# Optimization experiments

Measured on AMD Instinct MI355X. Metric: run time of the kernel, lower is better.

Reference implementation:

```python
import jax, jax.numpy as jnp
import numpy as np

NETWORK_MAP = {'DMN': [34, 35, 66, 67, 64, 65, 22, 23, 24, 25], 'SMN': [0, 1, 56, 57, 68, 69], 'VN': [42, 43, 44, 45, 46, 47, 48, 49, 50, 51, 52, 53], 'SN': [28, 29, 30, 31, 32, 33], 'FPN': [6, 7, 58, 59, 60, 61], 'LN': [36, 37, 38, 39, 40, 41], 'VAN': [10, 11, 14, 15], 'BGN': [70, 71, 72, 73, 74, 75, 76, 77], 'CereN': list(range(90, 116))}
N, K, B, IN_DIM, HID, HEADS = 116, 9, 512, 123, 128, 4
FLAT = K * HID + HID  # 1280


def _pool_mat():
    P = np.zeros((N, K), np.float32)
    for k, idxs in enumerate(NETWORK_MAP.values()):
        P[np.array(idxs), k] = 1.0
    return jnp.asarray(P)


def _bn(x, g, b, m, v):
    # eval-mode BatchNorm1d with running stats
    return (x - m) / jnp.sqrt(v + 1e-5) * g + b


def _gat(h, adj, W, a, g, bt, m, v):
    Bb, Nn, _ = h.shape
    H = a.shape[0]
    D = a.shape[1] // 2  # head_dim
    Wh = (h @ W).reshape(Bb, Nn, H, D)
    # additive GAT score factorization: (cat([Wh_i, Wh_j]) * a).sum(-1) = ei + ej
    ei = jnp.einsum('bnhd,hd->bnh', Wh, a[:, :D])
    ej = jnp.einsum('bnhd,hd->bnh', Wh, a[:, D:])
    e = ei[:, :, None, :] + ej[:, None, :, :]          # [B,N,N,H]
    e = jnp.where(e > 0, e, 0.2 * e)                   # leaky_relu(0.2)
    e = jnp.where((adj == 0)[..., None], -jnp.inf, e)  # mask non-edges
    attn = jax.nn.softmax(e, axis=2)                   # over neighbors j
    out = jnp.einsum('bijh,bjhd->bihd', attn, Wh).reshape(Bb, Nn, -1)
    out = _bn(out, g, bt, m, v)
    return jax.nn.elu(out) + h @ W


def setup_inputs() -> dict:
    key = jax.random.key(0)
    ks = jax.random.split(key, 24)
    f32 = jnp.float32

    def lin(k, fi, fo):
        return jax.random.normal(k, (fi, fo), f32) / np.sqrt(fi)

    x = jax.random.normal(ks[0], (B, N, IN_DIM), f32)
    adj = jax.random.randint(ks[1], (B, N, N), 0, 2).astype(f32)
    adj = jnp.maximum(adj, jnp.eye(N, dtype=f32)[None])  # self-loops
    return {
        'x': x, 'adj': adj,
        'W_enc': lin(ks[2], IN_DIM, HID), 'b_enc': jnp.zeros((HID,), f32),
        'bn_in_g': 1.0 + 0.1 * jax.random.normal(ks[3], (HID,), f32),
        'bn_in_b': 0.1 * jax.random.normal(ks[4], (HID,), f32),
        'bn_in_m': 0.05 * jax.random.normal(ks[5], (HID,), f32),
        'bn_in_v': jax.random.uniform(ks[6], (HID,), f32, 0.5, 1.5),
        'vne': 0.02 * jax.random.normal(ks[7], (1, 1, HID), f32),
        'W1': lin(ks[8], HID, HID),
        'a1': 0.1 * jax.random.normal(ks[9], (HEADS, 2 * (HID // HEADS)), f32),
        'g1': 1.0 + 0.1 * jax.random.normal(ks[10], (HID,), f32),
        'bt1': 0.1 * jax.random.normal(ks[11], (HID,), f32),
        'm1': 0.05 * jax.random.normal(ks[12], (HID,), f32),
        'v1': jax.random.uniform(ks[13], (HID,), f32, 0.5, 1.5),
        'W2': lin(ks[14], HID, HID),
        'a2': 0.1 * jax.random.normal(ks[15], (HEADS, 2 * (HID // HEADS)), f32),
        'g2': 1.0 + 0.1 * jax.random.normal(ks[16], (HID,), f32),
        'bt2': 0.1 * jax.random.normal(ks[17], (HID,), f32),
        'm2': 0.05 * jax.random.normal(ks[18], (HID,), f32),
        'v2': jax.random.uniform(ks[19], (HID,), f32, 0.5, 1.5),
        'Wv': lin(ks[20], 2 * HID, HID), 'bv': jnp.zeros((HID,), f32),
        'pool_mat': _pool_mat(),
        'Wa1': lin(ks[21], HID, 32), 'ba1': jnp.zeros((32,), f32),
        'Wa2': lin(ks[22], 32, 1), 'ba2': jnp.zeros((1,), f32),
        'ln_g': jnp.ones((FLAT,), f32), 'ln_b': jnp.zeros((FLAT,), f32),
        'Wc1': lin(ks[23], FLAT, 256), 'bc1': jnp.zeros((256,), f32),
        'Wc2': lin(jax.random.fold_in(key, 99), 256, 2), 'bc2': jnp.zeros((2,), f32),
    }


def reference(x, adj, W_enc, b_enc, bn_in_g, bn_in_b, bn_in_m, bn_in_v, vne,
              W1, a1, g1, bt1, m1, v1, W2, a2, g2, bt2, m2, v2,
              Wv, bv, pool_mat, Wa1, ba1, Wa2, ba2, ln_g, ln_b,
              Wc1, bc1, Wc2, bc2):
    Bb = x.shape[0]
    h = jax.nn.elu(x @ W_enc + b_enc)                 # node_encoder (dropout=eval)
    h = _bn(h, bn_in_g, bn_in_b, bn_in_m, bn_in_v)
    vn = vne + h.mean(axis=1, keepdims=True)          # [B,1,HID]
    h = _gat(h, adj, W1, a1, g1, bt1, m1, v1)
    vn_new = jax.nn.elu(jnp.concatenate([vn, h.mean(axis=1, keepdims=True)], -1) @ Wv + bv)
    h = h + vn_new * 0.1
    h2 = _gat(h, adj, W2, a2, g2, bt2, m2, v2)
    h = h2 + h
    vn = jax.nn.elu(jnp.concatenate([vn_new, h.mean(axis=1, keepdims=True)], -1) @ Wv + bv)
    pooled = jnp.einsum('bnd,nk->bkd', h, pool_mat)   # virtual-network pooling [B,K,HID]
    s = jnp.tanh(pooled @ Wa1 + ba1) @ Wa2 + ba2      # [B,K,1]
    net_w = jax.nn.softmax(s, axis=1)
    pooled = pooled * net_w
    flat = jnp.concatenate([pooled.reshape(Bb, -1), vn[:, 0]], axis=1)  # [B,FLAT]
    mu = flat.mean(axis=-1, keepdims=True)
    var = flat.var(axis=-1, keepdims=True)
    flat = (flat - mu) / jnp.sqrt(var + 1e-5) * ln_g + ln_b  # LayerNorm
    logits = jax.nn.elu(flat @ Wc1 + bc1) @ Wc2 + bc2        # classifier (dropout=eval)
    return (logits, flat)
```

## Files before the change

kernel.cpp:

```cpp
#include <hip/hip_runtime.h>
#include <hip/hip_bf16.h>
#include <math.h>

#define BATCH 512
#define N_NODES 116
#define IN_DIM 123
#define HID 128
#define HEADS 4
#define FLAT_DIM 1280

static constexpr int BN_TOT = BATCH * N_NODES;
static constexpr int HROW = N_NODES * HID;
static constexpr int ADJROW = N_NODES * N_NODES;

typedef short short8 __attribute__((ext_vector_type(8)));
typedef float f32x16 __attribute__((ext_vector_type(16)));

__device__ __forceinline__ float elu1(float x) {
    return x > 0.f ? x : __expf(x) - 1.f;
}
__device__ __forceinline__ short bfb(float x) {
    __hip_bfloat16 b = __float2bfloat16(x);
    return *reinterpret_cast<short*>(&b);
}

__global__ __launch_bounds__(256) void xprep_kernel(
    const float* __restrict__ x, short* __restrict__ xb)
{
    const int idx = blockIdx.x * 256 + threadIdx.x;
    const int row = idx >> 7, k = idx & 127;
    xb[idx] = (k < IN_DIM) ? bfb(x[(size_t)row * IN_DIM + k]) : (short)0;
}

__global__ __launch_bounds__(256) void wencprep_kernel(
    const float* __restrict__ W, short* __restrict__ Wb)
{
    const int idx = blockIdx.x * 256 + threadIdx.x;
    const int col = idx >> 7, k = idx & 127;
    Wb[idx] = (k < IN_DIM) ? bfb(W[(size_t)k * HID + col]) : (short)0;
}

__global__ __launch_bounds__(256) void enc_mfma(
    const short* __restrict__ xb, const short* __restrict__ Wencb,
    const float* __restrict__ bias,
    const float* __restrict__ g, const float* __restrict__ bta,
    const float* __restrict__ mn, const float* __restrict__ vr,
    float* __restrict__ hout)
{
    const int t = threadIdx.x;
    const int lane = t & 63, w = t >> 6;
    const int half = lane >> 5, nn = lane & 31;
    const int row0 = blockIdx.x * 128 + w * 32;
    const short8* ap = reinterpret_cast<const short8*>(xb + (size_t)(row0 + nn) * 128);
    short8 af[8];
#pragma unroll
    for (int s = 0; s < 8; ++s) af[s] = ap[s * 2 + half];
#pragma unroll
    for (int ct = 0; ct < 4; ++ct) {
        const int col = ct * 32 + nn;
        const short8* bp = reinterpret_cast<const short8*>(Wencb + (size_t)col * 128);
        f32x16 acc = {};
#pragma unroll
        for (int s = 0; s < 8; ++s)
            acc = __builtin_amdgcn_mfma_f32_32x32x16_bf16(af[s], bp[s * 2 + half], acc, 0, 0, 0);
        const float bb = bias[col];
        const float gg = g[col], bbn = bta[col], mm = mn[col];
        const float rstd = rsqrtf(vr[col] + 1e-5f);
#pragma unroll
        for (int reg = 0; reg < 16; ++reg) {
            const int r = (reg & 3) + 8 * (reg >> 2) + 4 * half;
            float val = elu1(acc[reg] + bb);
            val = (val - mm) * rstd * gg + bbn;
            hout[(size_t)(row0 + r) * HID + col] = val;
        }
    }
}

__global__ __launch_bounds__(256) void wprep_kernel(
    const float* __restrict__ W, const float* __restrict__ a,
    short* __restrict__ Wt, short* __restrict__ Weij)
{
    const int idx = blockIdx.x * 256 + threadIdx.x;
    const int h = idx >> 12, nn = (idx >> 7) & 31, k = idx & 127;
    Wt[idx] = bfb(W[k * HID + h * 32 + nn]);
    short wv = 0;
    if (nn < 2) {
        const float* ap = a + h * 64 + nn * 32;
        float s = 0.f;
#pragma unroll 8
        for (int d = 0; d < 32; ++d) s += W[k * HID + h * 32 + d] * ap[d];
        wv = bfb(s);
    }
    Weij[idx] = wv;
}

__global__ __launch_bounds__(256) void wc1prep_kernel(
    const float* __restrict__ Wc1, short* __restrict__ wc1t)
{
    const int idx = blockIdx.x * 256 + threadIdx.x;
    const int k = idx >> 8, n = idx & 255;
    wc1t[(size_t)n * FLAT_DIM + k] = bfb(Wc1[(size_t)k * 256 + n]);
}

__global__ __launch_bounds__(256) void adjpack_kernel(
    const float* __restrict__ adj, unsigned int* __restrict__ adjp)
{
    const int row = blockIdx.x * 4 + (threadIdx.x >> 6);
    const int l = threadIdx.x & 63;
    const float a1 = adj[(size_t)row * N_NODES + l];
    const float a2 = (l < N_NODES - 64) ? adj[(size_t)row * N_NODES + 64 + l] : 0.f;
    const unsigned long long m1 = __ballot(a1 != 0.f);
    const unsigned long long m2 = __ballot(a2 != 0.f);
    if (l == 0) {
        uint4 v;
        v.x = (unsigned int)m1; v.y = (unsigned int)(m1 >> 32);
        v.z = (unsigned int)m2; v.w = (unsigned int)(m2 >> 32);
        *reinterpret_cast<uint4*>(&adjp[(size_t)row * 4]) = v;
    }
}

template <bool ADD_H>
__global__ __launch_bounds__(256, 4) void gat_fused(
    const float* __restrict__ hin, float* __restrict__ hout,
    const short* __restrict__ Wt, const short* __restrict__ Weij,
    const unsigned int* __restrict__ adjp,
    const float* __restrict__ g, const float* __restrict__ bta,
    const float* __restrict__ mn, const float* __restrict__ vr,
    const float* __restrict__ vn, float* __restrict__ premean)
{
    constexpr int KP = 136;
    constexpr int WP = 33;
    __shared__ __align__(16) __hip_bfloat16 s_p[N_NODES][KP];
    __shared__ __align__(16) __hip_bfloat16 s_whsb[128][WP];
    __shared__ float s_eir[232];

    const int t = threadIdx.x;
    const int n_ = blockIdx.x;
    const int b = (n_ & 7) * 64 + (n_ >> 5);
    const int h = (n_ >> 3) & 3;

    const int lane = t & 63, w = t >> 6;
    const int half = lane >> 5, nn = lane & 31;

    {
        const int row = w * 32 + nn;
        const int hr = (row < N_NODES) ? row : 0;
        const float* hrow = hin + ((size_t)b * N_NODES + hr) * HID;
        const short8* wtp = reinterpret_cast<const short8*>(Wt + ((h * 32 + nn) << 7));
        const short8* wep = reinterpret_cast<const short8*>(Weij + ((h * 32 + nn) << 7));
        f32x16 wacc = {};
        f32x16 eacc = {};
#pragma unroll
        for (int s = 0; s < 8; ++s) {
            const int k0 = s * 16 + half * 8;
            float av[8];
            *reinterpret_cast<float4*>(&av[0]) = *reinterpret_cast<const float4*>(&hrow[k0]);
            *reinterpret_cast<float4*>(&av[4]) = *reinterpret_cast<const float4*>(&hrow[k0 + 4]);
            if (ADD_H) {
                float4 v0 = *reinterpret_cast<const float4*>(&vn[(size_t)b * HID + k0]);
                float4 v1 = *reinterpret_cast<const float4*>(&vn[(size_t)b * HID + k0 + 4]);
                av[0] += 0.1f * v0.x; av[1] += 0.1f * v0.y;
                av[2] += 0.1f * v0.z; av[3] += 0.1f * v0.w;
                av[4] += 0.1f * v1.x; av[5] += 0.1f * v1.y;
                av[6] += 0.1f * v1.z; av[7] += 0.1f * v1.w;
            }
            short8 afrag;
#pragma unroll
            for (int e = 0; e < 8; ++e) afrag[e] = bfb(av[e]);
            const int fi = s * 2 + half;
            wacc = __builtin_amdgcn_mfma_f32_32x32x16_bf16(afrag, wtp[fi], wacc, 0, 0, 0);
            eacc = __builtin_amdgcn_mfma_f32_32x32x16_bf16(afrag, wep[fi], eacc, 0, 0, 0);
        }
#pragma unroll
        for (int reg = 0; reg < 16; ++reg) {
            const int r = (reg & 3) + 8 * (reg >> 2) + 4 * half;
            s_whsb[w * 32 + r][nn] = __float2bfloat16(wacc[reg]);
        }
        if (nn == 0) {
#pragma unroll
            for (int reg = 0; reg < 16; ++reg) {
                const int r = w * 32 + (reg & 3) + 8 * (reg >> 2) + 4 * half;
                if (r < N_NODES) s_eir[r] = eacc[reg];
            }
        }
        if (nn == 1) {
#pragma unroll
            for (int reg = 0; reg < 16; ++reg) {
                const int r = w * 32 + (reg & 3) + 8 * (reg >> 2) + 4 * half;
                if (r < N_NODES) s_eir[N_NODES + r] = eacc[reg];
            }
        }
    }
    __syncthreads();

    {
        const int l = lane;
        const float ejl = s_eir[N_NODES + l];
        const bool up = (l < N_NODES - 64);
        const float ejl2 = up ? s_eir[N_NODES + l + 64] : 0.f;
        const int i0 = w * 32;
        const int cnt = min(32, N_NODES - i0);
        const uint4* ap = reinterpret_cast<const uint4*>(
            adjp + ((size_t)b * N_NODES + i0) * 4);
        uint4 aw = ap[0];
        for (int ii = 0; ii < cnt; ++ii) {
            uint4 nw = aw;
            if (ii + 1 < cnt) nw = ap[ii + 1];
            const int i = i0 + ii;
            const float eii = s_eir[i];
            const unsigned int w1 = (l & 32) ? aw.y : aw.x;
            const unsigned int w2 = (l & 32) ? aw.w : aw.z;
            const bool bit1 = (w1 >> (l & 31)) & 1;
            const bool bit2 = (w2 >> (l & 31)) & 1;
            float e1 = eii + ejl;
            e1 = e1 > 0.f ? e1 : 0.2f * e1;
            const float x1 = bit1 ? __expf(e1) : 0.f;
            float x2 = 0.f;
            if (up) {
                float e2 = eii + ejl2;
                e2 = e2 > 0.f ? e2 : 0.2f * e2;
                x2 = bit2 ? __expf(e2) : 0.f;
            }
            s_p[i][l] = __float2bfloat16(x1);
            s_p[i][l + 64] = __float2bfloat16(x2);
            aw = nw;
        }
    }

    float psum = 0.f;
    {
        f32x16 acc = {};
        f32x16 accs = {};
        short8 ones;
#pragma unroll
        for (int e = 0; e < 8; ++e) ones[e] = (short)0x3F80;
#pragma unroll
        for (int s = 0; s < 8; ++s) {
            const int k0 = s * 16 + half * 8;
            const short8 afrag = *reinterpret_cast<const short8*>(
                &s_p[0][0] + (size_t)(w * 32 + nn) * KP + k0);
            short8 bfrag;
#pragma unroll
            for (int e = 0; e < 8; ++e)
                bfrag[e] = *reinterpret_cast<const short*>(&s_whsb[k0 + e][nn]);
            acc = __builtin_amdgcn_mfma_f32_32x32x16_bf16(afrag, bfrag, acc, 0, 0, 0);
            accs = __builtin_amdgcn_mfma_f32_32x32x16_bf16(afrag, ones, accs, 0, 0, 0);
        }
        const int f = h * 32 + nn;
        const float gg = g[f], bb = bta[f], mm = mn[f];
        const float rstd = rsqrtf(vr[f] + 1e-5f);
        const float vadd = ADD_H ? 0.1f * vn[(size_t)b * HID + f] : 0.f;
#pragma unroll
        for (int reg = 0; reg < 16; ++reg) {
            const int row = (reg & 3) + 8 * (reg >> 2) + 4 * half;
            const int i = w * 32 + row;
            if (i < N_NODES) {
                const size_t off = ((size_t)b * N_NODES + i) * HID + f;
                const float aval = acc[reg] / accs[reg];
                float xv = elu1((aval - mm) * rstd * gg + bb);
                float outv = xv + __bfloat162float(s_whsb[i][nn]);
                if (ADD_H) outv += hin[off] + vadd;
                hout[off] = outv;
                psum += outv;
            }
        }
    }
    psum += __shfl_xor(psum, 32);
    __syncthreads();
    if (half == 0) s_eir[w * 32 + nn] = psum;
    __syncthreads();
    if (t < 32) {
        const float s = s_eir[t] + s_eir[32 + t] + s_eir[64 + t] + s_eir[96 + t];
        premean[(size_t)b * HID + h * 32 + t] = s * (1.f / N_NODES);
    }
}

__global__ __launch_bounds__(128) void vn0_kernel(
    const float* __restrict__ h, const float* __restrict__ vne,
    float* __restrict__ vn)
{
    const int b = blockIdx.x, f = threadIdx.x;
    float s = 0.f;
    for (int n = 0; n < N_NODES; ++n) s += h[(size_t)b * HROW + n * HID + f];
    vn[b * HID + f] = vne[f] + s * (1.f / N_NODES);
}

__global__ __launch_bounds__(128) void vn_mlp_kernel(
    const float* __restrict__ prev, const float* __restrict__ premean,
    const float* __restrict__ Wv, const float* __restrict__ bv,
    float* __restrict__ vout)
{
    __shared__ float cat[2 * HID];
    const int b = blockIdx.x, f = threadIdx.x;
    cat[f] = prev[b * HID + f];
    cat[HID + f] = premean[b * HID + f];
    __syncthreads();
    float acc = bv[f];
    for (int k = 0; k < 2 * HID; ++k) acc += cat[k] * Wv[k * HID + f];
    vout[b * HID + f] = elu1(acc);
}

__global__ __launch_bounds__(128) void pool_flat_kernel(
    const float* __restrict__ h, const float* __restrict__ vnf,
    const float* __restrict__ pm,
    const float* __restrict__ Wa1, const float* __restrict__ ba1,
    const float* __restrict__ Wa2, const float* __restrict__ ba2,
    const float* __restrict__ ln_g, const float* __restrict__ ln_b,
    float* __restrict__ out, short* __restrict__ flatb)
{
    __shared__ float s_pm[N_NODES * 9];
    __shared__ float s_p[9][HID];
    __shared__ float s_s[9];
    __shared__ float s_red[4];
    const int b = blockIdx.x, f = threadIdx.x;
    for (int idx = f; idx < N_NODES * 9; idx += 128) s_pm[idx] = pm[idx];
    float p[9] = {};
    __syncthreads();
    for (int n = 0; n < N_NODES; ++n) {
        const float hv = h[(size_t)b * HROW + n * HID + f];
#pragma unroll
        for (int k = 0; k < 9; ++k) p[k] += s_pm[n * 9 + k] * hv;
    }
#pragma unroll
    for (int k = 0; k < 9; ++k) s_p[k][f] = p[k];
    __syncthreads();
    for (int pass = 0; pass < 3; ++pass) {
        const int k = pass * 4 + (f >> 5);
        if (k < 9) {
            const int j = f & 31;
            float z = ba1[j];
            for (int d = 0; d < HID; ++d) z += s_p[k][d] * Wa1[d * 32 + j];
            z = tanhf(z);
            float part = z * Wa2[j];
#pragma unroll
            for (int off = 16; off; off >>= 1) part += __shfl_xor(part, off);
            if (j == 0) s_s[k] = part + ba2[0];
        }
    }
    __syncthreads();
    float smax = -1e30f;
#pragma unroll
    for (int k = 0; k < 9; ++k) smax = fmaxf(smax, s_s[k]);
    float wgt[9], ssum = 0.f;
#pragma unroll
    for (int k = 0; k < 9; ++k) { wgt[k] = expf(s_s[k] - smax); ssum += wgt[k]; }
    const float sinv = 1.f / ssum;
    float vals[10];
#pragma unroll
    for (int k = 0; k < 9; ++k) vals[k] = p[k] * wgt[k] * sinv;
    vals[9] = vnf[b * HID + f];
    float lsum = 0.f, lsq = 0.f;
#pragma unroll
    for (int q = 0; q < 10; ++q) { lsum += vals[q]; lsq += vals[q] * vals[q]; }
#pragma unroll
    for (int off = 32; off; off >>= 1) {
        lsum += __shfl_xor(lsum, off);
        lsq += __shfl_xor(lsq, off);
    }
    const int lane = f & 63, wid = f >> 6;
    if (lane == 0) { s_red[wid * 2] = lsum; s_red[wid * 2 + 1] = lsq; }
    __syncthreads();
    const float tot = s_red[0] + s_red[2];
    const float totsq = s_red[1] + s_red[3];
    const float mean = tot * (1.f / FLAT_DIM);
    const float var = totsq * (1.f / FLAT_DIM) - mean * mean;
    const float rstd = rsqrtf(var + 1e-5f);
    float* fout = out + 1024 + (size_t)b * FLAT_DIM;
    short* fb = flatb + (size_t)b * FLAT_DIM;
#pragma unroll
    for (int k = 0; k < 9; ++k) {
        const int j = k * HID + f;
        const float v = (vals[k] - mean) * rstd * ln_g[j] + ln_b[j];
        fout[j] = v;
        fb[j] = bfb(v);
    }
    const int j = 9 * HID + f;
    const float v9 = (vals[9] - mean) * rstd * ln_g[j] + ln_b[j];
    fout[j] = v9;
    fb[j] = bfb(v9);
}

__global__ __launch_bounds__(256) void cls_mm_kernel(
// ... 2 lines not shown
{
    const int t = threadIdx.x;
    const int lane = t & 63, w = t >> 6;
    const int half = lane >> 5, nn = lane & 31;
    const int mt = blockIdx.x >> 1;
    const int nh = blockIdx.x & 1;
    const int r0 = mt * 32;
    const int c0 = nh * 128 + w * 32;
    const short8* ap = reinterpret_cast<const short8*>(flatb + (size_t)(r0 + nn) * FLAT_DIM);
    const short8* bp = reinterpret_cast<const short8*>(wc1t + (size_t)(c0 + nn) * FLAT_DIM);
    f32x16 acc = {};
#pragma unroll 8
    for (int s = 0; s < 80; ++s) {
        const int fi = s * 2 + half;
        acc = __builtin_amdgcn_mfma_f32_32x32x16_bf16(ap[fi], bp[fi], acc, 0, 0, 0);
    }
    const float bb = bc1[c0 + nn];
#pragma unroll
    for (int reg = 0; reg < 16; ++reg) {
        const int row = (reg & 3) + 8 * (reg >> 2) + 4 * half;
        hid[(size_t)(r0 + row) * 256 + c0 + nn] = elu1(acc[reg] + bb);
    }
}

__global__ __launch_bounds__(256) void logits_kernel(
    const float* __restrict__ hid, const float* __restrict__ Wc2,
    const float* __restrict__ bc2, float* __restrict__ out)
{
    const int idx = blockIdx.x * 256 + threadIdx.x;
    const int row = idx >> 1, c = idx & 1;
    const float4* hp = reinterpret_cast<const float4*>(hid + (size_t)row * 256);
    float acc = 0.f;
#pragma unroll 8
    for (int q = 0; q < 64; ++q) {
        const float4 hv = hp[q];
        acc += hv.x * Wc2[(q * 4 + 0) * 2 + c] + hv.y * Wc2[(q * 4 + 1) * 2 + c]
             + hv.z * Wc2[(q * 4 + 2) * 2 + c] + hv.w * Wc2[(q * 4 + 3) * 2 + c];
    }
    out[idx] = acc + bc2[c];
}

extern "C" void kernel_launch(void* const* d_in, const int* in_sizes, int n_in,
                              void* d_out, int out_size, void* d_ws, size_t ws_size,
                              hipStream_t stream)
{
    const float* x     = (const float*)d_in[0];
    const float* adj   = (const float*)d_in[1];
    const float* W_enc = (const float*)d_in[2];
    const float* b_enc = (const float*)d_in[3];
    const float* bn_g  = (const float*)d_in[4];
    const float* bn_b  = (const float*)d_in[5];
    const float* bn_m  = (const float*)d_in[6];
    const float* bn_v  = (const float*)d_in[7];
    const float* vne   = (const float*)d_in[8];
    const float* W1    = (const float*)d_in[9];
    const float* a1    = (const float*)d_in[10];
    const float* g1    = (const float*)d_in[11];
    const float* bt1   = (const float*)d_in[12];
    const float* m1    = (const float*)d_in[13];
    const float* v1    = (const float*)d_in[14];
    const float* W2    = (const float*)d_in[15];
    const float* a2    = (const float*)d_in[16];
    const float* g2    = (const float*)d_in[17];
    const float* bt2   = (const float*)d_in[18];
    const float* m2    = (const float*)d_in[19];
    const float* v2    = (const float*)d_in[20];
    const float* Wv    = (const float*)d_in[21];
    const float* bv    = (const float*)d_in[22];
    const float* pm    = (const float*)d_in[23];
    const float* Wa1   = (const float*)d_in[24];
    const float* ba1   = (const float*)d_in[25];
    const float* Wa2   = (const float*)d_in[26];
    const float* ba2   = (const float*)d_in[27];
    const float* ln_g  = (const float*)d_in[28];
    const float* ln_b  = (const float*)d_in[29];
    const float* Wc1   = (const float*)d_in[30];
    const float* bc1   = (const float*)d_in[31];
    const float* Wc2   = (const float*)d_in[32];
    const float* bc2   = (const float*)d_in[33];
    float* out = (float*)d_out;

    float* ws = (float*)d_ws;
    float* hA   = ws;
    float* hB   = hA + (size_t)BN_TOT * HID;
    float* vn0  = hB + (size_t)BN_TOT * HID;
    float* vnn  = vn0 + BATCH * HID;
    float* vnf  = vnn + BATCH * HID;
    float* pms1 = vnf + BATCH * HID;
    float* pms2 = pms1 + BATCH * HID;
    unsigned int* adjp = (unsigned int*)(pms2 + BATCH * HID);
    short* Wt1  = (short*)(adjp + (size_t)BN_TOT * 4);
    short* We1  = Wt1 + 16384;
    short* Wt2  = We1 + 16384;
    short* We2  = Wt2 + 16384;
    short* Wencb = We2 + 16384;
    short* xb    = (short*)hB;
    short* flatb = (short*)hB;
    short* wc1t  = flatb + (size_t)BATCH * FLAT_DIM;
    float* hid   = (float*)(wc1t + 256 * FLAT_DIM);

    wprep_kernel<<<64, 256, 0, stream>>>(W1, a1, Wt1, We1);
    wprep_kernel<<<64, 256, 0, stream>>>(W2, a2, Wt2, We2);
    wencprep_kernel<<<64, 256, 0, stream>>>(W_enc, Wencb);
    adjpack_kernel<<<BN_TOT / 4, 256, 0, stream>>>(adj, adjp);
    xprep_kernel<<<BN_TOT * 128 / 256, 256, 0, stream>>>(x, xb);

    enc_mfma<<<BN_TOT / 128, 256, 0, stream>>>(xb, Wencb, b_enc, bn_g, bn_b,
                                               bn_m, bn_v, hA);
    vn0_kernel<<<BATCH, 128, 0, stream>>>(hA, vne, vn0);
    gat_fused<false><<<BATCH * HEADS, 256, 0, stream>>>(
        hA, hB, Wt1, We1, adjp, g1, bt1, m1, v1, nullptr, pms1);
    vn_mlp_kernel<<<BATCH, 128, 0, stream>>>(vn0, pms1, Wv, bv, vnn);
    gat_fused<true><<<BATCH * HEADS, 256, 0, stream>>>(
        hB, hA, Wt2, We2, adjp, g2, bt2, m2, v2, vnn, pms2);
    vn_mlp_kernel<<<BATCH, 128, 0, stream>>>(vnn, pms2, Wv, bv, vnf);
    wc1prep_kernel<<<1280, 256, 0, stream>>>(Wc1, wc1t);
    pool_flat_kernel<<<BATCH, 128, 0, stream>>>(hA, vnf, pm, Wa1, ba1, Wa2, ba2,
                                                ln_g, ln_b, out, flatb);
    cls_mm_kernel<<<32, 256, 0, stream>>>(flatb, wc1t, bc1, hid);
    logits_kernel<<<4, 256, 0, stream>>>(hid, Wc2, bc2, out);
}
```

Measured before the change: 239.7 us.

## Fuse both GAT layers, all heads and virtual-node MLPs into one per-batch kernel

Replaces the two per-(batch,head) GAT launches and two vn_mlp launches with a single kernel that has one block per batch sample. The block loops over both layers and all four heads, keeps the input A-fragments in registers, caches the adjacency bitmask in shared memory, and computes the virtual-node MLP in-block. The intermediate layer-1 output is stored as bf16. This removes launch overhead and the fp32 round trips of the intermediate h. The trade-off is only 512 blocks with serialized heads, which lowers parallelism, and bf16 storage of the intermediate adds rounding error.

```diff
diff --git a/kernel.cpp b/kernel.cpp
--- a/kernel.cpp
+++ b/kernel.cpp
@@ -11,7 +11,6 @@
 
 static constexpr int BN_TOT = BATCH * N_NODES;
 static constexpr int HROW = N_NODES * HID;
-static constexpr int ADJROW = N_NODES * N_NODES;
 
 typedef short short8 __attribute__((ext_vector_type(8)));
 typedef float f32x16 __attribute__((ext_vector_type(16)));
@@ -22,6 +21,9 @@
 __device__ __forceinline__ short bfb(float x) {
     __hip_bfloat16 b = __float2bfloat16(x);
     return *reinterpret_cast<short*>(&b);
+}
+__device__ __forceinline__ float bf2f(short s) {
+    return __bfloat162float(*reinterpret_cast<__hip_bfloat16*>(&s));
 }
 
 __global__ __launch_bounds__(256) void xprep_kernel(
@@ -119,185 +121,210 @@
     }
 }
 
-template <bool ADD_H>
-__global__ __launch_bounds__(256, 4) void gat_fused(
-    const float* __restrict__ hin, float* __restrict__ hout,
-    const short* __restrict__ Wt, const short* __restrict__ Weij,
-    const unsigned int* __restrict__ adjp,
-    const float* __restrict__ g, const float* __restrict__ bta,
-    const float* __restrict__ mn, const float* __restrict__ vr,
-    const float* __restrict__ vn, float* __restrict__ premean)
+__global__ __launch_bounds__(128) void vn0_kernel(
+    const float* __restrict__ h, const float* __restrict__ vne,
+    float* __restrict__ vn)
+{
+    const int b = blockIdx.x, f = threadIdx.x;
+    float s = 0.f;
+    for (int n = 0; n < N_NODES; ++n) s += h[(size_t)b * HROW + n * HID + f];
+    vn[b * HID + f] = vne[f] + s * (1.f / N_NODES);
+}
+
+__global__ __launch_bounds__(256, 3) void gat_mega(
+    float* __restrict__ hA,
+    short* __restrict__ hb1,
+    const short* __restrict__ Wt1, const short* __restrict__ We1,
+    const short* __restrict__ Wt2, const short* __restrict__ We2,
+    const uint4* __restrict__ adjp4,
+    const float* __restrict__ g1, const float* __restrict__ bt1,
+    const float* __restrict__ m1, const float* __restrict__ v1,
+    const float* __restrict__ g2, const float* __restrict__ bt2,
+    const float* __restrict__ m2, const float* __restrict__ v2,
+    const float* __restrict__ vn0g, const float* __restrict__ Wv,
+    const float* __restrict__ bv, float* __restrict__ vnfg)
 {
     constexpr int KP = 136;
     constexpr int WP = 33;
     __shared__ __align__(16) __hip_bfloat16 s_p[N_NODES][KP];
     __shared__ __align__(16) __hip_bfloat16 s_whsb[128][WP];
+    __shared__ uint4 s_adj[N_NODES];
     __shared__ float s_eir[232];
+    __shared__ float s_vn[128];
+    __shared__ float s_pm[128];
+    __shared__ float s_red[128];
 
     const int t = threadIdx.x;
-    const int n_ = blockIdx.x;
-    const int b = (n_ & 7) * 64 + (n_ >> 5);
-    const int h = (n_ >> 3) & 3;
-
+    const int b = blockIdx.x;
     const int lane = t & 63, w = t >> 6;
     const int half = lane >> 5, nn = lane & 31;
-
+    const int row = w * 32 + nn;
+    const int hr = (row < N_NODES) ? row : 0;
+
+    if (t < N_NODES) s_adj[t] = adjp4[(size_t)b * N_NODES + t];
+    if (t < 128) s_vn[t] = vn0g[(size_t)b * 128 + t];
+
+    short8 af[8];
     {
-        const int row = w * 32 + nn;
-        const int hr = (row < N_NODES) ? row : 0;
-        const float* hrow = hin + ((size_t)b * N_NODES + hr) * HID;
-        const short8* wtp = reinterpret_cast<const short8*>(Wt + ((h * 32 + nn) << 7));
-        const short8* wep = reinterpret_cast<const short8*>(Weij + ((h * 32 + nn) << 7));
-        f32x16 wacc = {};
-        f32x16 eacc = {};
+        const float* hrow = hA + ((size_t)b * N_NODES + hr) * HID;
 #pragma unroll
         for (int s = 0; s < 8; ++s) {
             const int k0 = s * 16 + half * 8;
-            float av[8];
-            *reinterpret_cast<float4*>(&av[0]) = *reinterpret_cast<const float4*>(&hrow[k0]);
-            *reinterpret_cast<float4*>(&av[4]) = *reinterpret_cast<const float4*>(&hrow[k0 + 4]);
-            if (ADD_H) {
-                float4 v0 = *reinterpret_cast<const float4*>(&vn[(size_t)b * HID + k0]);
-                float4 v1 = *reinterpret_cast<const float4*>(&vn[(size_t)b * HID + k0 + 4]);
-                av[0] += 0.1f * v0.x; av[1] += 0.1f * v0.y;
-                av[2] += 0.1f * v0.z; av[3] += 0.1f * v0.w;
-                av[4] += 0.1f * v1.x; av[5] += 0.1f * v1.y;
-                av[6] += 0.1f * v1.z; av[7] += 0.1f * v1.w;
-            }
-            short8 afrag;
-#pragma unroll
-            for (int e = 0; e < 8; ++e) afrag[e] = bfb(av[e]);
-            const int fi = s * 2 + half;
-            wacc = __builtin_amdgcn_mfma_f32_32x32x16_bf16(afrag, wtp[fi], wacc, 0, 0, 0);
-            eacc = __builtin_amdgcn_mfma_f32_32x32x16_bf16(afrag, wep[fi], eacc, 0, 0, 0);
+            const float4 x0 = *reinterpret_cast<const float4*>(&hrow[k0]);
+            const float4 x1 = *reinterpret_cast<const float4*>(&hrow[k0 + 4]);
+            short8 fr;
+            fr[0] = bfb(x0.x); fr[1] = bfb(x0.y); fr[2] = bfb(x0.z); fr[3] = bfb(x0.w);
+            fr[4] = bfb(x1.x); fr[5] = bfb(x1.y); fr[6] = bfb(x1.z); fr[7] = bfb(x1.w);
+            af[s] = fr;
         }
-#pragma unroll
-        for (int reg = 0; reg < 16; ++reg) {
-            const int r = (reg & 3) + 8 * (reg >> 2) + 4 * half;
-            s_whsb[w * 32 + r][nn] = __float2bfloat16(wacc[reg]);
+    }
+
+    for (int L = 0; L < 2; ++L) {
+        const short* Wt = L ? Wt2 : Wt1;
+        const short* We = L ? We2 : We1;
+        const float* g_ = L ? g2 : g1;   const float* bt_ = L ? bt2 : bt1;
+        const float* mn_ = L ? m2 : m1;  const float* vr_ = L ? v2 : v1;
+
+        for (int h = 0; h < HEADS; ++h) {
+            const short8* wtp = reinterpret_cast<const short8*>(Wt + ((h * 32 + nn) << 7));
+            const short8* wep = reinterpret_cast<const short8*>(We + ((h * 32 + nn) << 7));
+            f32x16 wacc = {};
+            f32x16 eacc = {};
+#pragma unroll
+            for (int s = 0; s < 8; ++s) {
+                const int fi = s * 2 + half;
+                wacc = __builtin_amdgcn_mfma_f32_32x32x16_bf16(af[s], wtp[fi], wacc, 0, 0, 0);
+                eacc = __builtin_amdgcn_mfma_f32_32x32x16_bf16(af[s], wep[fi], eacc, 0, 0, 0);
+            }
+            __syncthreads();
+#pragma unroll
+            for (int reg = 0; reg < 16; ++reg) {
+                const int r = (reg & 3) + 8 * (reg >> 2) + 4 * half;
+                s_whsb[w * 32 + r][nn] = __float2bfloat16(wacc[reg]);
+            }
+            if (nn == 0) {
+#pragma unroll
+                for (int reg = 0; reg < 16; ++reg) {
+                    const int r = w * 32 + (reg & 3) + 8 * (reg >> 2) + 4 * half;
+                    if (r < N_NODES) s_eir[r] = eacc[reg];
+                }
+            }
+            if (nn == 1) {
+#pragma unroll
+                for (int reg = 0; reg < 16; ++reg) {
+                    const int r = w * 32 + (reg & 3) + 8 * (reg >> 2) + 4 * half;
+                    if (r < N_NODES) s_eir[N_NODES + r] = eacc[reg];
+                }
+            }
+            __syncthreads();
+
+            {
+                const int l = lane;
+                const float ejl = s_eir[N_NODES + l];
+                const bool up = (l < N_NODES - 64);
+                const float ejl2 = up ? s_eir[N_NODES + l + 64] : 0.f;
+                const int i0 = w * 32;
+                const int cnt = min(32, N_NODES - i0);
+                for (int ii = 0; ii < cnt; ++ii) {
+                    const int i = i0 + ii;
+                    const uint4 aw = s_adj[i];
+                    const float eii = s_eir[i];
+                    const unsigned int w1 = (l & 32) ? aw.y : aw.x;
+                    const unsigned int w2 = (l & 32) ? aw.w : aw.z;
+                    const bool bit1 = (w1 >> (l & 31)) & 1;
+                    const bool bit2 = (w2 >> (l & 31)) & 1;
+                    float e1 = eii + ejl;
+                    e1 = e1 > 0.f ? e1 : 0.2f * e1;
+                    const float x1 = bit1 ? __expf(e1) : 0.f;
+                    float x2 = 0.f;
+                    if (up) {
+                        float e2 = eii + ejl2;
+                        e2 = e2 > 0.f ? e2 : 0.2f * e2;
+                        x2 = bit2 ? __expf(e2) : 0.f;
+                    }
+                    s_p[i][l] = __float2bfloat16(x1);
+                    s_p[i][l + 64] = __float2bfloat16(x2);
+                }
+            }
+
+            float psum = 0.f;
+            {
+                f32x16 acc = {};
+                f32x16 accs = {};
+                short8 ones;
+#pragma unroll
+                for (int e = 0; e < 8; ++e) ones[e] = (short)0x3F80;
+#pragma unroll
+                for (int s = 0; s < 8; ++s) {
+                    const int k0 = s * 16 + half * 8;
+                    const short8 afr = *reinterpret_cast<const short8*>(
+                        &s_p[0][0] + (size_t)row * KP + k0);
+                    short8 bfr;
+#pragma unroll
+                    for (int e = 0; e < 8; ++e)
+                        bfr[e] = *reinterpret_cast<const short*>(&s_whsb[k0 + e][nn]);
+                    acc = __builtin_amdgcn_mfma_f32_32x32x16_bf16(afr, bfr, acc, 0, 0, 0);
+                    accs = __builtin_amdgcn_mfma_f32_32x32x16_bf16(afr, ones, accs, 0, 0, 0);
+                }
+                const int f = h * 32 + nn;
+                const float G = g_[f], B = bt_[f], M = mn_[f];
+                const float R = rsqrtf(vr_[f] + 1e-5f);
+#pragma unroll
+                for (int reg = 0; reg < 16; ++reg) {
+                    const int r = (reg & 3) + 8 * (reg >> 2) + 4 * half;
+                    const int i = w * 32 + r;
+                    if (i < N_NODES) {
+                        const size_t off = ((size_t)b * N_NODES + i) * HID + f;
+                        const float aval = acc[reg] / accs[reg];
+                        float xv = elu1((aval - M) * R * G + B);
+                        float outv = xv + bf2f(*reinterpret_cast<const short*>(&s_whsb[i][nn]));
+                        if (L == 1) {
+                            outv += bf2f(hb1[off]) + 0.1f * s_vn[f];
+                            hA[off] = outv;
+                        } else {
+                            hb1[off] = bfb(outv);
+                        }
+                        psum += outv;
+                    }
+                }
+            }
+            psum += __shfl_xor(psum, 32);
+            if (half == 0) s_red[w * 32 + nn] = psum;
+            __syncthreads();
+            if (t < 32)
+                s_pm[h * 32 + t] = (s_red[t] + s_red[32 + t] + s_red[64 + t]
+                                    + s_red[96 + t]) * (1.f / N_NODES);
         }
-        if (nn == 0) {
-#pragma unroll
-            for (int reg = 0; reg < 16; ++reg) {
-                const int r = w * 32 + (reg & 3) + 8 * (reg >> 2) + 4 * half;
-                if (r < N_NODES) s_eir[r] = eacc[reg];
-            }
+
+        __syncthreads();
+        float vval = 0.f;
+        if (t < 128) {
+            float acc2 = bv[t];
+#pragma unroll 4
+            for (int k = 0; k < 128; ++k) acc2 += s_vn[k] * Wv[k * HID + t];
+#pragma unroll 4
+            for (int k = 0; k < 128; ++k) acc2 += s_pm[k] * Wv[(128 + k) * HID + t];
+            vval = elu1(acc2);
         }
-        if (nn == 1) {
-#pragma unroll
-            for (int reg = 0; reg < 16; ++reg) {
-                const int r = w * 32 + (reg & 3) + 8 * (reg >> 2) + 4 * half;
-                if (r < N_NODES) s_eir[N_NODES + r] = eacc[reg];
-            }
+        __syncthreads();
+        if (L == 0) {
+            if (t < 128) s_vn[t] = vval;
+            __syncthreads();
+            const short* hbrow = hb1 + ((size_t)b * N_NODES + hr) * HID;
+#pragma unroll
+            for (int s = 0; s < 8; ++s) {
+                const int k0 = s * 16 + half * 8;
+                const short8 v = *reinterpret_cast<const short8*>(&hbrow[k0]);
+                short8 fr;
+#pragma unroll
+                for (int e = 0; e < 8; ++e)
+                    fr[e] = bfb(bf2f(v[e]) + 0.1f * s_vn[k0 + e]);
+                af[s] = fr;
+            }
+        } else {
+            if (t < 128) vnfg[(size_t)b * HID + t] = vval;
         }
     }
-    __syncthreads();
-
-    {
-        const int l = lane;
-        const float ejl = s_eir[N_NODES + l];
-        const bool up = (l < N_NODES - 64);
-        const float ejl2 = up ? s_eir[N_NODES + l + 64] : 0.f;
-        const int i0 = w * 32;
-        const int cnt = min(32, N_NODES - i0);
-        const uint4* ap = reinterpret_cast<const uint4*>(
-            adjp + ((size_t)b * N_NODES + i0) * 4);
-        uint4 aw = ap[0];
-        for (int ii = 0; ii < cnt; ++ii) {
-            uint4 nw = aw;
-            if (ii + 1 < cnt) nw = ap[ii + 1];
-            const int i = i0 + ii;
-            const float eii = s_eir[i];
-            const unsigned int w1 = (l & 32) ? aw.y : aw.x;
-            const unsigned int w2 = (l & 32) ? aw.w : aw.z;
-            const bool bit1 = (w1 >> (l & 31)) & 1;
-            const bool bit2 = (w2 >> (l & 31)) & 1;
-            float e1 = eii + ejl;
-            e1 = e1 > 0.f ? e1 : 0.2f * e1;
-            const float x1 = bit1 ? __expf(e1) : 0.f;
-            float x2 = 0.f;
-            if (up) {
-                float e2 = eii + ejl2;
-                e2 = e2 > 0.f ? e2 : 0.2f * e2;
-                x2 = bit2 ? __expf(e2) : 0.f;
-            }
-            s_p[i][l] = __float2bfloat16(x1);
-            s_p[i][l + 64] = __float2bfloat16(x2);
-            aw = nw;
-        }
-    }
-
-    float psum = 0.f;
-    {
-        f32x16 acc = {};
-        f32x16 accs = {};
-        short8 ones;
-#pragma unroll
-        for (int e = 0; e < 8; ++e) ones[e] = (short)0x3F80;
-#pragma unroll
-        for (int s = 0; s < 8; ++s) {
-            const int k0 = s * 16 + half * 8;
-            const short8 afrag = *reinterpret_cast<const short8*>(
-                &s_p[0][0] + (size_t)(w * 32 + nn) * KP + k0);
-            short8 bfrag;
-#pragma unroll
-            for (int e = 0; e < 8; ++e)
-                bfrag[e] = *reinterpret_cast<const short*>(&s_whsb[k0 + e][nn]);
-            acc = __builtin_amdgcn_mfma_f32_32x32x16_bf16(afrag, bfrag, acc, 0, 0, 0);
-            accs = __builtin_amdgcn_mfma_f32_32x32x16_bf16(afrag, ones, accs, 0, 0, 0);
-        }
-        const int f = h * 32 + nn;
-        const float gg = g[f], bb = bta[f], mm = mn[f];
-        const float rstd = rsqrtf(vr[f] + 1e-5f);
-        const float vadd = ADD_H ? 0.1f * vn[(size_t)b * HID + f] : 0.f;
-#pragma unroll
-        for (int reg = 0; reg < 16; ++reg) {
-            const int row = (reg & 3) + 8 * (reg >> 2) + 4 * half;
-            const int i = w * 32 + row;
-            if (i < N_NODES) {
-                const size_t off = ((size_t)b * N_NODES + i) * HID + f;
-                const float aval = acc[reg] / accs[reg];
-                float xv = elu1((aval - mm) * rstd * gg + bb);
-                float outv = xv + __bfloat162float(s_whsb[i][nn]);
-                if (ADD_H) outv += hin[off] + vadd;
-                hout[off] = outv;
-                psum += outv;
-            }
-        }
-    }
-    psum += __shfl_xor(psum, 32);
-    __syncthreads();
-    if (half == 0) s_eir[w * 32 + nn] = psum;
-    __syncthreads();
-    if (t < 32) {
-        const float s = s_eir[t] + s_eir[32 + t] + s_eir[64 + t] + s_eir[96 + t];
-        premean[(size_t)b * HID + h * 32 + t] = s * (1.f / N_NODES);
-    }
-}
-
-__global__ __launch_bounds__(128) void vn0_kernel(
-    const float* __restrict__ h, const float* __restrict__ vne,
-    float* __restrict__ vn)
-{
-    const int b = blockIdx.x, f = threadIdx.x;
-    float s = 0.f;
-    for (int n = 0; n < N_NODES; ++n) s += h[(size_t)b * HROW + n * HID + f];
-    vn[b * HID + f] = vne[f] + s * (1.f / N_NODES);
-}
-
-__global__ __launch_bounds__(128) void vn_mlp_kernel(
-    const float* __restrict__ prev, const float* __restrict__ premean,
-    const float* __restrict__ Wv, const float* __restrict__ bv,
-    float* __restrict__ vout)
-{
-    __shared__ float cat[2 * HID];
-    const int b = blockIdx.x, f = threadIdx.x;
-    cat[f] = prev[b * HID + f];
-    cat[HID + f] = premean[b * HID + f];
-    __syncthreads();
-    float acc = bv[f];
-    for (int k = 0; k < 2 * HID; ++k) acc += cat[k] * Wv[k * HID + f];
-    vout[b * HID + f] = elu1(acc);
 }
 
 __global__ __launch_bounds__(128) void pool_flat_kernel(
@@ -467,18 +494,16 @@
     float* ws = (float*)d_ws;
     float* hA   = ws;
     float* hB   = hA + (size_t)BN_TOT * HID;
-    float* vn0  = hB + (size_t)BN_TOT * HID;
-    float* vnn  = vn0 + BATCH * HID;
-    float* vnf  = vnn + BATCH * HID;
-    float* pms1 = vnf + BATCH * HID;
-    float* pms2 = pms1 + BATCH * HID;
-    unsigned int* adjp = (unsigned int*)(pms2 + BATCH * HID);
+    float* vn0g = hB + (size_t)BN_TOT * HID;
+    float* vnfg = vn0g + BATCH * HID;
+    unsigned int* adjp = (unsigned int*)(vnfg + BATCH * HID);
     short* Wt1  = (short*)(adjp + (size_t)BN_TOT * 4);
     short* We1  = Wt1 + 16384;
     short* Wt2  = We1 + 16384;
     short* We2  = Wt2 + 16384;
     short* Wencb = We2 + 16384;
     short* xb    = (short*)hB;
+    short* hb1   = (short*)hB;
     short* flatb = (short*)hB;
     short* wc1t  = flatb + (size_t)BATCH * FLAT_DIM;
     float* hid   = (float*)(wc1t + 256 * FLAT_DIM);
@@ -491,15 +516,12 @@
 
     enc_mfma<<<BN_TOT / 128, 256, 0, stream>>>(xb, Wencb, b_enc, bn_g, bn_b,
                                                bn_m, bn_v, hA);
-    vn0_kernel<<<BATCH, 128, 0, stream>>>(hA, vne, vn0);
-    gat_fused<false><<<BATCH * HEADS, 256, 0, stream>>>(
-        hA, hB, Wt1, We1, adjp, g1, bt1, m1, v1, nullptr, pms1);
-    vn_mlp_kernel<<<BATCH, 128, 0, stream>>>(vn0, pms1, Wv, bv, vnn);
-    gat_fused<true><<<BATCH * HEADS, 256, 0, stream>>>(
-        hB, hA, Wt2, We2, adjp, g2, bt2, m2, v2, vnn, pms2);
-    vn_mlp_kernel<<<BATCH, 128, 0, stream>>>(vnn, pms2, Wv, bv, vnf);
+    vn0_kernel<<<BATCH, 128, 0, stream>>>(hA, vne, vn0g);
+    gat_mega<<<BATCH, 256, 0, stream>>>(
+        hA, hb1, Wt1, We1, Wt2, We2, (const uint4*)adjp,
+        g1, bt1, m1, v1, g2, bt2, m2, v2, vn0g, Wv, bv, vnfg);
     wc1prep_kernel<<<1280, 256, 0, stream>>>(Wc1, wc1t);
-    pool_flat_kernel<<<BATCH, 128, 0, stream>>>(hA, vnf, pm, Wa1, ba1, Wa2, ba2,
+    pool_flat_kernel<<<BATCH, 128, 0, stream>>>(hA, vnfg, pm, Wa1, ba1, Wa2, ba2,
                                                 ln_g, ln_b, out, flatb);
     cls_mm_kernel<<<32, 256, 0, stream>>>(flatb, wc1t, bc1, hid);
     logits_kernel<<<4, 256, 0, stream>>>(hid, Wc2, bc2, out);
```

After: 244.8 us. 2.1% more time.

## Store intermediate node features in bf16, fold virtual-node add algebraically, merge prep kernels

Applied to the files above, without the earlier changes.

The encoder output and the first GAT layer output are now stored as bf16 instead of fp32, which halves their global traffic and lets the GAT prologue feed MFMA fragments directly without converting. The virtual-node broadcast add before layer 2 is moved out of the per-node input: its product with W2 and with the attention vectors is precomputed per batch in the vn MLP kernel and added as a correction. The five prep kernels are merged into one launch. The cost is extra rounding from storing h in bf16 and a slight reordering of where the rounding happens.

```diff
diff --git a/kernel.cpp b/kernel.cpp
--- a/kernel.cpp
+++ b/kernel.cpp
@@ -11,7 +11,6 @@
 
 static constexpr int BN_TOT = BATCH * N_NODES;
 static constexpr int HROW = N_NODES * HID;
-static constexpr int ADJROW = N_NODES * N_NODES;
 
 typedef short short8 __attribute__((ext_vector_type(8)));
 typedef float f32x16 __attribute__((ext_vector_type(16)));
@@ -23,21 +22,74 @@
     __hip_bfloat16 b = __float2bfloat16(x);
     return *reinterpret_cast<short*>(&b);
 }
-
-__global__ __launch_bounds__(256) void xprep_kernel(
-    const float* __restrict__ x, short* __restrict__ xb)
+__device__ __forceinline__ float bf2f(short s) {
+    return __bfloat162float(*reinterpret_cast<__hip_bfloat16*>(&s));
+}
+
+__global__ __launch_bounds__(256) void prep_all(
+    const float* __restrict__ x, const float* __restrict__ adj,
+    const float* __restrict__ W_enc,
+    const float* __restrict__ W1, const float* __restrict__ a1,
+    const float* __restrict__ W2, const float* __restrict__ a2,
+    short* __restrict__ xb, unsigned int* __restrict__ adjp,
+    short* __restrict__ Wencb,
+    short* __restrict__ Wt1, short* __restrict__ We1,
+    short* __restrict__ Wt2, short* __restrict__ We2)
+{
+    const int blk = blockIdx.x, t = threadIdx.x;
+    if (blk < 128) {
+        const float* W = (blk < 64) ? W1 : W2;
+        const float* a = (blk < 64) ? a1 : a2;
+        short* Wt = (blk < 64) ? Wt1 : Wt2;
+        short* We = (blk < 64) ? We1 : We2;
+        const int idx = (blk & 63) * 256 + t;
+        const int h = idx >> 12, nn = (idx >> 7) & 31, k = idx & 127;
+        Wt[idx] = bfb(W[k * HID + h * 32 + nn]);
+        short wv = 0;
+        if (nn < 2) {
+            const float* ap = a + h * 64 + nn * 32;
+            float s = 0.f;
+#pragma unroll 8
+            for (int d = 0; d < 32; ++d) s += W[k * HID + h * 32 + d] * ap[d];
+            wv = bfb(s);
+        }
+        We[idx] = wv;
+    } else if (blk < 192) {
+        const int idx = (blk - 128) * 256 + t;
+        const int col = idx >> 7, k = idx & 127;
+        Wencb[idx] = (k < IN_DIM) ? bfb(W_enc[(size_t)k * HID + col]) : (short)0;
+    } else if (blk < 192 + BN_TOT / 4) {
+        const int row = (blk - 192) * 4 + (t >> 6);
+        const int l = t & 63;
+        const float v1 = adj[(size_t)row * N_NODES + l];
+        const float v2 = (l < N_NODES - 64) ? adj[(size_t)row * N_NODES + 64 + l] : 0.f;
+        const unsigned long long m1 = __ballot(v1 != 0.f);
+        const unsigned long long m2 = __ballot(v2 != 0.f);
+        if (l == 0) {
+            uint4 v;
+            v.x = (unsigned int)m1; v.y = (unsigned int)(m1 >> 32);
+            v.z = (unsigned int)m2; v.w = (unsigned int)(m2 >> 32);
+            *reinterpret_cast<uint4*>(&adjp[(size_t)row * 4]) = v;
+        }
+    } else {
+        const int i = (blk - (192 + BN_TOT / 4)) * 256 + t;
+        const int row = i >> 4, kb = (i & 15) * 8;
+        short8 v;
+#pragma unroll
+        for (int e = 0; e < 8; ++e) {
+            const int k = kb + e;
+            v[e] = (k < IN_DIM) ? bfb(x[(size_t)row * IN_DIM + k]) : (short)0;
+        }
+        *reinterpret_cast<short8*>(&xb[(size_t)row * 128 + kb]) = v;
+    }
+}
+
+__global__ __launch_bounds__(256) void wc1prep_kernel(
+    const float* __restrict__ Wc1, short* __restrict__ wc1t)
 {
     const int idx = blockIdx.x * 256 + threadIdx.x;
-    const int row = idx >> 7, k = idx & 127;
-    xb[idx] = (k < IN_DIM) ? bfb(x[(size_t)row * IN_DIM + k]) : (short)0;
-}
-
-__global__ __launch_bounds__(256) void wencprep_kernel(
-    const float* __restrict__ W, short* __restrict__ Wb)
-{
-    const int idx = blockIdx.x * 256 + threadIdx.x;
-    const int col = idx >> 7, k = idx & 127;
-    Wb[idx] = (k < IN_DIM) ? bfb(W[(size_t)k * HID + col]) : (short)0;
+    const int k = idx >> 8, n = idx & 255;
+    wc1t[(size_t)n * FLAT_DIM + k] = bfb(Wc1[(size_t)k * 256 + n]);
 }
 
 __global__ __launch_bounds__(256) void enc_mfma(
@@ -45,7 +97,7 @@
     const float* __restrict__ bias,
     const float* __restrict__ g, const float* __restrict__ bta,
     const float* __restrict__ mn, const float* __restrict__ vr,
-    float* __restrict__ hout)
+    short* __restrict__ houtb)
 {
     const int t = threadIdx.x;
     const int lane = t & 63, w = t >> 6;
@@ -71,62 +123,32 @@
             const int r = (reg & 3) + 8 * (reg >> 2) + 4 * half;
             float val = elu1(acc[reg] + bb);
             val = (val - mm) * rstd * gg + bbn;
-            hout[(size_t)(row0 + r) * HID + col] = val;
-        }
-    }
-}
-
-__global__ __launch_bounds__(256) void wprep_kernel(
-    const float* __restrict__ W, const float* __restrict__ a,
-    short* __restrict__ Wt, short* __restrict__ Weij)
-{
-    const int idx = blockIdx.x * 256 + threadIdx.x;
-    const int h = idx >> 12, nn = (idx >> 7) & 31, k = idx & 127;
-    Wt[idx] = bfb(W[k * HID + h * 32 + nn]);
-    short wv = 0;
-    if (nn < 2) {
-        const float* ap = a + h * 64 + nn * 32;
-        float s = 0.f;
-#pragma unroll 8
-        for (int d = 0; d < 32; ++d) s += W[k * HID + h * 32 + d] * ap[d];
-        wv = bfb(s);
-    }
-    Weij[idx] = wv;
-}
-
-__global__ __launch_bounds__(256) void wc1prep_kernel(
-    const float* __restrict__ Wc1, short* __restrict__ wc1t)
-{
-    const int idx = blockIdx.x * 256 + threadIdx.x;
-    const int k = idx >> 8, n = idx & 255;
-    wc1t[(size_t)n * FLAT_DIM + k] = bfb(Wc1[(size_t)k * 256 + n]);
-}
-
-__global__ __launch_bounds__(256) void adjpack_kernel(
-    const float* __restrict__ adj, unsigned int* __restrict__ adjp)
-{
-    const int row = blockIdx.x * 4 + (threadIdx.x >> 6);
-    const int l = threadIdx.x & 63;
-    const float a1 = adj[(size_t)row * N_NODES + l];
-    const float a2 = (l < N_NODES - 64) ? adj[(size_t)row * N_NODES + 64 + l] : 0.f;
-    const unsigned long long m1 = __ballot(a1 != 0.f);
-    const unsigned long long m2 = __ballot(a2 != 0.f);
-    if (l == 0) {
-        uint4 v;
-        v.x = (unsigned int)m1; v.y = (unsigned int)(m1 >> 32);
-        v.z = (unsigned int)m2; v.w = (unsigned int)(m2 >> 32);
-        *reinterpret_cast<uint4*>(&adjp[(size_t)row * 4]) = v;
-    }
-}
-
-template <bool ADD_H>
+            houtb[(size_t)(row0 + r) * HID + col] = bfb(val);
+        }
+    }
+}
+
+__global__ __launch_bounds__(128) void vn0_kernel(
+    const short* __restrict__ hb, const float* __restrict__ vne,
+    float* __restrict__ vn)
+{
+    const int b = blockIdx.x, f = threadIdx.x;
+    float s = 0.f;
+    for (int n = 0; n < N_NODES; ++n)
+        s += bf2f(hb[(size_t)(b * N_NODES + n) * HID + f]);
+    vn[b * HID + f] = vne[f] + s * (1.f / N_NODES);
+}
+
+template <int L>
 __global__ __launch_bounds__(256, 4) void gat_fused(
-    const float* __restrict__ hin, float* __restrict__ hout,
+    const short* __restrict__ hbin, short* __restrict__ houtb,
+    float* __restrict__ houtf,
     const short* __restrict__ Wt, const short* __restrict__ Weij,
     const unsigned int* __restrict__ adjp,
-    const float* __restrict__ g, const float* __restrict__ bta,
-    const float* __restrict__ mn, const float* __restrict__ vr,
-    const float* __restrict__ vn, float* __restrict__ premean)
+    const float* __restrict__ g_, const float* __restrict__ bt_,
+    const float* __restrict__ mn_, const float* __restrict__ vr_,
+    const float* __restrict__ vn, const float* __restrict__ wcorr,
+    const float* __restrict__ eicorr, float* __restrict__ premean)
 {
     constexpr int KP = 136;
     constexpr int WP = 33;
@@ -141,35 +163,29 @@
 
     const int lane = t & 63, w = t >> 6;
     const int half = lane >> 5, nn = lane & 31;
+    const int row = w * 32 + nn;
+    const int hr = (row < N_NODES) ? row : 0;
+
+    float wc = 0.f, eic = 0.f, ejc = 0.f;
+    if (L == 1) {
+        wc = wcorr[(size_t)b * HID + h * 32 + nn];
+        eic = eicorr[b * 8 + h * 2];
+        ejc = eicorr[b * 8 + h * 2 + 1];
+    }
 
     {
-        const int row = w * 32 + nn;
-        const int hr = (row < N_NODES) ? row : 0;
-        const float* hrow = hin + ((size_t)b * N_NODES + hr) * HID;
+        const short8* ap = reinterpret_cast<const short8*>(
+            hbin + (size_t)(b * N_NODES + hr) * HID);
         const short8* wtp = reinterpret_cast<const short8*>(Wt + ((h * 32 + nn) << 7));
         const short8* wep = reinterpret_cast<const short8*>(Weij + ((h * 32 + nn) << 7));
         f32x16 wacc = {};
         f32x16 eacc = {};
 #pragma unroll
         for (int s = 0; s < 8; ++s) {
-            const int k0 = s * 16 + half * 8;
-            float av[8];
-            *reinterpret_cast<float4*>(&av[0]) = *reinterpret_cast<const float4*>(&hrow[k0]);
-            *reinterpret_cast<float4*>(&av[4]) = *reinterpret_cast<const float4*>(&hrow[k0 + 4]);
-            if (ADD_H) {
-                float4 v0 = *reinterpret_cast<const float4*>(&vn[(size_t)b * HID + k0]);
-                float4 v1 = *reinterpret_cast<const float4*>(&vn[(size_t)b * HID + k0 + 4]);
-                av[0] += 0.1f * v0.x; av[1] += 0.1f * v0.y;
-                av[2] += 0.1f * v0.z; av[3] += 0.1f * v0.w;
-                av[4] += 0.1f * v1.x; av[5] += 0.1f * v1.y;
-                av[6] += 0.1f * v1.z; av[7] += 0.1f * v1.w;
-            }
-            short8 afrag;
-#pragma unroll
-            for (int e = 0; e < 8; ++e) afrag[e] = bfb(av[e]);
             const int fi = s * 2 + half;
-            wacc = __builtin_amdgcn_mfma_f32_32x32x16_bf16(afrag, wtp[fi], wacc, 0, 0, 0);
-            eacc = __builtin_amdgcn_mfma_f32_32x32x16_bf16(afrag, wep[fi], eacc, 0, 0, 0);
+            const short8 af = ap[fi];
+            wacc = __builtin_amdgcn_mfma_f32_32x32x16_bf16(af, wtp[fi], wacc, 0, 0, 0);
+            eacc = __builtin_amdgcn_mfma_f32_32x32x16_bf16(af, wep[fi], eacc, 0, 0, 0);
         }
 #pragma unroll
         for (int reg = 0; reg < 16; ++reg) {
@@ -180,14 +196,14 @@
 #pragma unroll
             for (int reg = 0; reg < 16; ++reg) {
                 const int r = w * 32 + (reg & 3) + 8 * (reg >> 2) + 4 * half;
-                if (r < N_NODES) s_eir[r] = eacc[reg];
+                if (r < N_NODES) s_eir[r] = eacc[reg] + eic;
             }
         }
         if (nn == 1) {
 #pragma unroll
             for (int reg = 0; reg < 16; ++reg) {
                 const int r = w * 32 + (reg & 3) + 8 * (reg >> 2) + 4 * half;
-                if (r < N_NODES) s_eir[N_NODES + r] = eacc[reg];
+                if (r < N_NODES) s_eir[N_NODES + r] = eacc[reg] + ejc;
             }
         }
     }
@@ -238,7 +254,7 @@
         for (int s = 0; s < 8; ++s) {
             const int k0 = s * 16 + half * 8;
             const short8 afrag = *reinterpret_cast<const short8*>(
-                &s_p[0][0] + (size_t)(w * 32 + nn) * KP + k0);
+                &s_p[0][0] + (size_t)row * KP + k0);
             short8 bfrag;
 #pragma unroll
             for (int e = 0; e < 8; ++e)
@@ -247,20 +263,24 @@
             accs = __builtin_amdgcn_mfma_f32_32x32x16_bf16(afrag, ones, accs, 0, 0, 0);
         }
         const int f = h * 32 + nn;
-        const float gg = g[f], bb = bta[f], mm = mn[f];
-        const float rstd = rsqrtf(vr[f] + 1e-5f);
-        const float vadd = ADD_H ? 0.1f * vn[(size_t)b * HID + f] : 0.f;
+        const float G = g_[f], B = bt_[f], M = mn_[f];
+        const float R = rsqrtf(vr_[f] + 1e-5f);
+        const float vadd = (L == 1) ? 0.1f * vn[(size_t)b * HID + f] : 0.f;
 #pragma unroll
         for (int reg = 0; reg < 16; ++reg) {
-            const int row = (reg & 3) + 8 * (reg >> 2) + 4 * half;
-            const int i = w * 32 + row;
+            const int r = (reg & 3) + 8 * (reg >> 2) + 4 * half;
+            const int i = w * 32 + r;
             if (i < N_NODES) {
                 const size_t off = ((size_t)b * N_NODES + i) * HID + f;
-                const float aval = acc[reg] / accs[reg];
-                float xv = elu1((aval - mm) * rstd * gg + bb);
-                float outv = xv + __bfloat162float(s_whsb[i][nn]);
-                if (ADD_H) outv += hin[off] + vadd;
-                hout[off] = outv;
+                const float aval = acc[reg] / accs[reg] + wc;
+                float xv = elu1((aval - M) * R * G + B);
+                float outv = xv + bf2f(*reinterpret_cast<const short*>(&s_whsb[i][nn])) + wc;
+                if (L == 1) {
+                    outv += bf2f(hbin[off]) + vadd;
+                    houtf[off] = outv;
+                } else {
+                    houtb[off] = bfb(outv);
+                }
                 psum += outv;
             }
         }
@@ -275,20 +295,13 @@
     }
 }
 
-__global__ __launch_bounds__(128) void vn0_kernel(
-    const float* __restrict__ h, const float* __restrict__ vne,
-    float* __restrict__ vn)
-{
-    const int b = blockIdx.x, f = threadIdx.x;
-    float s = 0.f;
-    for (int n = 0; n < N_NODES; ++n) s += h[(size_t)b * HROW + n * HID + f];
-    vn[b * HID + f] = vne[f] + s * (1.f / N_NODES);
-}
-
+template <bool EMIT>
 __global__ __launch_bounds__(128) void vn_mlp_kernel(
     const float* __restrict__ prev, const float* __restrict__ premean,
     const float* __restrict__ Wv, const float* __restrict__ bv,
-    float* __restrict__ vout)
+    const float* __restrict__ W2, const float* __restrict__ a2,
+    float* __restrict__ vout, float* __restrict__ wcorr,
+    float* __restrict__ eicorr)
 {
     __shared__ float cat[2 * HID];
     const int b = blockIdx.x, f = threadIdx.x;
@@ -297,7 +310,29 @@
     __syncthreads();
     float acc = bv[f];
     for (int k = 0; k < 2 * HID; ++k) acc += cat[k] * Wv[k * HID + f];
-    vout[b * HID + f] = elu1(acc);
+    const float o = elu1(acc);
+    vout[b * HID + f] = o;
+    if (EMIT) {
+        __syncthreads();
+        cat[f] = o;
+        __syncthreads();
+        float wcf = 0.f;
+#pragma unroll 4
+        for (int k = 0; k < HID; ++k) wcf += cat[k] * W2[k * HID + f];
+        wcf *= 0.1f;
+        wcorr[(size_t)b * HID + f] = wcf;
+        __syncthreads();
+        cat[f] = wcf;
+        __syncthreads();
+        if (f < 8) {
+            const int h = f >> 1, sel = f & 1;
+            float e = 0.f;
+#pragma unroll 8
+            for (int d = 0; d < 32; ++d)
+                e += cat[h * 32 + d] * a2[h * 64 + sel * 32 + d];
+            eicorr[b * 8 + f] = e;
+        }
+    }
 }
 
 __global__ __launch_bounds__(128) void pool_flat_kernel(
@@ -466,38 +501,43 @@
 
     float* ws = (float*)d_ws;
     float* hA   = ws;
-    float* hB   = hA + (size_t)BN_TOT * HID;
-    float* vn0  = hB + (size_t)BN_TOT * HID;
-    float* vnn  = vn0 + BATCH * HID;
+    short* hb0  = (short*)(hA + (size_t)BN_TOT * HID);
+    short* h1b  = hb0 + (size_t)BN_TOT * HID;
+    float* tail = (float*)(h1b + (size_t)BN_TOT * HID);
+    float* vn0g = tail;
+    float* vnn  = vn0g + BATCH * HID;
     float* vnf  = vnn + BATCH * HID;
     float* pms1 = vnf + BATCH * HID;
     float* pms2 = pms1 + BATCH * HID;
-    unsigned int* adjp = (unsigned int*)(pms2 + BATCH * HID);
+    float* wcorr = pms2 + BATCH * HID;
+    float* eicorr = wcorr + BATCH * HID;
+    unsigned int* adjp = (unsigned int*)(eicorr + BATCH * 8);
     short* Wt1  = (short*)(adjp + (size_t)BN_TOT * 4);
     short* We1  = Wt1 + 16384;
     short* Wt2  = We1 + 16384;
     short* We2  = Wt2 + 16384;
     short* Wencb = We2 + 16384;
-    short* xb    = (short*)hB;
-    short* flatb = (short*)hB;
-    short* wc1t  = flatb + (size_t)BATCH * FLAT_DIM;
+    short* xb    = h1b;
+    short* flatb = hb0;
+    short* wc1t  = h1b;
     float* hid   = (float*)(wc1t + 256 * FLAT_DIM);
 
-    wprep_kernel<<<64, 256, 0, stream>>>(W1, a1, Wt1, We1);
-    wprep_kernel<<<64, 256, 0, stream>>>(W2, a2, Wt2, We2);
-    wencprep_kernel<<<64, 256, 0, stream>>>(W_enc, Wencb);
-    adjpack_kernel<<<BN_TOT / 4, 256, 0, stream>>>(adj, adjp);
-    xprep_kernel<<<BN_TOT * 128 / 256, 256, 0, stream>>>(x, xb);
-
+    const int prep_blocks = 192 + BN_TOT / 4 + (BN_TOT * 16) / 256;
+    prep_all<<<prep_blocks, 256, 0, stream>>>(x, adj, W_enc, W1, a1, W2, a2,
+                                              xb, adjp, Wencb, Wt1, We1, Wt2, We2);
     enc_mfma<<<BN_TOT / 128, 256, 0, stream>>>(xb, Wencb, b_enc, bn_g, bn_b,
-                                               bn_m, bn_v, hA);
-    vn0_kernel<<<BATCH, 128, 0, stream>>>(hA, vne, vn0);
-    gat_fused<false><<<BATCH * HEADS, 256, 0, stream>>>(
-        hA, hB, Wt1, We1, adjp, g1, bt1, m1, v1, nullptr, pms1);
-    vn_mlp_kernel<<<BATCH, 128, 0, stream>>>(vn0, pms1, Wv, bv, vnn);
-    gat_fused<true><<<BATCH * HEADS, 256, 0, stream>>>(
-        hB, hA, Wt2, We2, adjp, g2, bt2, m2, v2, vnn, pms2);
-    vn_mlp_kernel<<<BATCH, 128, 0, stream>>>(vnn, pms2, Wv, bv, vnf);
+                                               bn_m, bn_v, hb0);
+    vn0_kernel<<<BATCH, 128, 0, stream>>>(hb0, vne, vn0g);
+    gat_fused<0><<<BATCH * HEADS, 256, 0, stream>>>(
+        hb0, h1b, nullptr, Wt1, We1, adjp, g1, bt1, m1, v1,
+        nullptr, nullptr, nullptr, pms1);
+    vn_mlp_kernel<true><<<BATCH, 128, 0, stream>>>(vn0g, pms1, Wv, bv, W2, a2,
+                                                   vnn, wcorr, eicorr);
+    gat_fused<1><<<BATCH * HEADS, 256, 0, stream>>>(
+        h1b, nullptr, hA, Wt2, We2, adjp, g2, bt2, m2, v2,
+        vnn, wcorr, eicorr, pms2);
+    vn_mlp_kernel<false><<<BATCH, 128, 0, stream>>>(vnn, pms2, Wv, bv, nullptr,
+                                                    nullptr, vnf, nullptr, nullptr);
     wc1prep_kernel<<<1280, 256, 0, stream>>>(Wc1, wc1t);
     pool_flat_kernel<<<BATCH, 128, 0, stream>>>(hA, vnf, pm, Wa1, ba1, Wa2, ba2,
                                                 ln_g, ln_b, out, flatb);
```

Measured after the change: 219.2 us. -8.6%, faster.
